# Kernel tuning notes

Measured on AMD Instinct MI355X. Metric: run time of the kernel, lower is better.

## Reference

```python
import jax, jax.numpy as jnp
from jax import lax
import numpy as np
import math

EPS = 1e-5
NBINS = 17   # quantized color levels round(x*255/16) for x in [0,1)
K_MODE = 11

def _bn(x, g, b):
    # BatchNorm2d in training mode: batch statistics over (B,H,W)
    m = jnp.mean(x, axis=(0, 2, 3), keepdims=True)
    v = jnp.var(x, axis=(0, 2, 3), keepdims=True)
    return (x - m) * lax.rsqrt(v + EPS) * g[None, :, None, None] + b[None, :, None, None]

def _lrelu(x):
    return jnp.where(x >= 0, x, 0.01 * x)

def _shared_conv(x, w, b, stride, padding):
    # one KxK kernel shared depthwise across all channels, scalar bias
    C = x.shape[1]
    k = jnp.tile(w[None, None], (C, 1, 1, 1))  # (C,1,K,K)
    y = lax.conv_general_dilated(x, k, (stride, stride),
                                 [(padding, padding), (padding, padding)],
                                 dimension_numbers=('NCHW', 'OIHW', 'NCHW'),
                                 feature_group_count=C)
    return y + b[0]

def _avg_pool_same(x, k):
    # avg_pool2d(k, stride=1, padding=k//2, count_include_pad=True)
    p = k // 2
    s = lax.reduce_window(x, 0.0, lax.add, (1, 1, k, k), (1, 1, 1, 1),
                          [(0, 0), (0, 0), (p, p), (p, p)])
    return s / float(k * k)

def _mode_pool(xq):
    # xq values are exact multiples of 16/256 -> recover integer bin index,
    # then mode over 11x11 window = argmax of per-bin counts (histogram).
    # torch zero-padding corresponds to bin 0; argmax first-max tie-break ->
    # smallest value, matching torch.mode.
    q = jnp.clip(jnp.round(xq * (256.0 / 16.0)).astype(jnp.int32), 0, NBINS - 1)
    pad = K_MODE // 2
    qp = jnp.pad(q, ((0, 0), (0, 0), (pad, pad), (pad, pad)))
    onehot = (qp[:, :, None] == jnp.arange(NBINS, dtype=jnp.int32)[None, None, :, None, None]).astype(jnp.float32)
    counts = lax.reduce_window(onehot, 0.0, lax.add, (1, 1, 1, K_MODE, K_MODE), (1, 1, 1, 1, 1), 'VALID')
    mode_bin = jnp.argmax(counts, axis=2)  # (B,C,H,W)
    return mode_bin.astype(xq.dtype) * (16.0 / 256.0)

def _forward(x, p_w1, p_b1, p_dw1, p_db1, p_g1, p_be1,
             p_w2, p_b2, p_dw2, p_db2, p_g2, p_be2,
             d_w, d_b, ia_w, ia_b, ia_g, ia_be,
             ib_w, ib_b, ib_g, ib_be,
             f_g1, f_be1, f_g2, f_be2):
    xq = jnp.round(x * (255.0 / 16.0)) * (16.0 / 256.0)
    xm = _mode_pool(xq)
    B, C, H, W = xm.shape
    half = p_w1.shape[0]

    # prepare: 1x1 conv -> depthwise 1x1 (per-channel scale) -> BN -> LeakyReLU, twice
    h = jnp.einsum('bchw,oc->bohw', xm, p_w1) + p_b1[None, :, None, None]
    h = h * p_dw1[None, :, None, None] + p_db1[None, :, None, None]
    h = _lrelu(_bn(h, p_g1, p_be1))
    h = jnp.einsum('bchw,oc->bohw', h, p_w2) + p_b2[None, :, None, None]
    h = h * p_dw2[None, :, None, None] + p_db2[None, :, None, None]
    h = _lrelu(_bn(h, p_g2, p_be2))

    n = int(math.floor(math.log(min(H, W), 3)))
    score = jnp.zeros((B, 2 * half, H, W), x.dtype)
    d = h
    for _ in range(n):
        d = _shared_conv(d, d_w, d_b, 3, 1)  # stride-3 downgrade
        z = jax.image.resize(d, (B, half, H, W), method='bilinear')
        a = _lrelu(_bn(_shared_conv(z, ia_w, ia_b, 1, 2), ia_g, ia_be))
        bb = _lrelu(_bn(_shared_conv(z, ib_w, ib_b, 1, 2), ib_g, ib_be))
        score = score + jnp.concatenate([a, bb], axis=1)  # Splitter + Stack(1)

    def ft(s):
        s = _bn(s, f_g1, f_be1)
        s = jnp.where(s > 0.1, 0.1 + 0.7 * (s - 0.1), s)  # MaxLeakyReLU(0.7, 0.1)
        s = _bn(s, f_g2, f_be2)
        return 2.0 * s - _avg_pool_same(s, K_MODE)  # EmphaseLocal(11): x + (x - local mean)

    score = ft(ft(ft(score)))
    return score / n

def setup_inputs() -> dict:
    key = jax.random.key(0)
    ks = jax.random.split(key, 32)
    B, Cin, H, W, half = 8, 3, 384, 384, 32
    r = lambda i, shp, s=0.1: s * jax.random.normal(ks[i], shp, dtype=jnp.float32)
    g = lambda i, shp: 1.0 + 0.1 * jax.random.normal(ks[i], shp, dtype=jnp.float32)
    return dict(
        x=jax.random.uniform(ks[0], (B, Cin, H, W), dtype=jnp.float32),
        p_w1=r(1, (half, Cin), 0.3), p_b1=r(2, (half,)),
        p_dw1=g(3, (half,)), p_db1=r(4, (half,)),
        p_g1=g(5, (half,)), p_be1=r(6, (half,)),
        p_w2=r(7, (half, half), 0.2), p_b2=r(8, (half,)),
        p_dw2=g(9, (half,)), p_db2=r(10, (half,)),
        p_g2=g(11, (half,)), p_be2=r(12, (half,)),
        d_w=r(13, (3, 3), 0.2), d_b=r(14, (1,)),
        ia_w=r(15, (5, 5), 0.2), ia_b=r(16, (1,)),
        ia_g=g(17, (half,)), ia_be=r(18, (half,)),
        ib_w=r(19, (5, 5), 0.2), ib_b=r(20, (1,)),
        ib_g=g(21, (half,)), ib_be=r(22, (half,)),
        f_g1=g(23, (2 * half,)), f_be1=r(24, (2 * half,)),
        f_g2=g(25, (2 * half,)), f_be2=r(26, (2 * half,)),
    )

def reference(x, p_w1, p_b1, p_dw1, p_db1, p_g1, p_be1,
              p_w2, p_b2, p_dw2, p_db2, p_g2, p_be2,
              d_w, d_b, ia_w, ia_b, ia_g, ia_be,
              ib_w, ib_b, ib_g, ib_be,
              f_g1, f_be1, f_g2, f_be2):
    return _forward(x, p_w1, p_b1, p_dw1, p_db1, p_g1, p_be1,
                    p_w2, p_b2, p_dw2, p_db2, p_g2, p_be2,
                    d_w, d_b, ia_w, ia_b, ia_g, ia_be,
                    ib_w, ib_b, ib_g, ib_be,
                    f_g1, f_be1, f_g2, f_be2)
```

## Files before the change

kernel.cpp:

```cpp
#include <hip/hip_runtime.h>

#define HW 147456
#define WID 384
#define NB 8
#define NPC 1179648
#define HW4 36864

static __device__ __forceinline__ float lrelu01(float v) { return v >= 0.f ? v : 0.01f * v; }
static __device__ __forceinline__ float mlrelu(float v) { return v > 0.1f ? 0.1f + 0.7f * (v - 0.1f) : v; }

__global__ __launch_bounds__(256) void mode_kernel(const float* __restrict__ x,
                                                   float* __restrict__ xm) {
  __shared__ unsigned char qt[26 * 76];
  __shared__ unsigned int cc[16 * 5 * 76];
  const int plane = blockIdx.z;
  const int x0 = blockIdx.x * 64;
  const int y0 = blockIdx.y * 16;
  const float* xp = x + (size_t)plane * HW;

  for (int i = threadIdx.x; i < 26 * 76; i += 256) {
    int r = i / 76, ccol = i - r * 76;
    int gy = y0 + r - 5, gx = x0 + ccol - 5;
    unsigned char q = 0;
    if (ccol < 74 && gy >= 0 && gy < WID && gx >= 0 && gx < WID) {
// ... 113 lines not shown
    double e2 = (a0 * a0 * M[3] + a1 * a1 * M[6] + a2 * a2 * M[8] +
                 2.0 * (a0 * a1 * M[4] + a0 * a2 * M[5] + a1 * a2 * M[7])) / N +
                2.0 * k * lin + k * k;
    double var = e2 - mean * mean;
    float rstd = rsqrtf((float)var + 1e-5f);
    float scl = rstd * g[o];
    sc[o] = scl;
    sh[o] = be[o] - (float)mean * scl;
  }
}

__global__ __launch_bounds__(256) void prep_fused(const float* __restrict__ xm,
                                                  const float* __restrict__ w1,
                                                  const float* __restrict__ b1,
                                                  const float* __restrict__ dw1,
                                                  const float* __restrict__ db1,
                                                  const float* __restrict__ P1SC,
                                                  const float* __restrict__ P1SH,
                                                  const float* __restrict__ w2,
                                                  const float* __restrict__ b2,
                                                  const float* __restrict__ dw2,
                                                  const float* __restrict__ db2,
                                                  float* __restrict__ t2,
                                                  float* __restrict__ part) {
  __shared__ float wl[1024];
  __shared__ float c1[32][4];
  __shared__ float bias2[32];
  __shared__ float wred[8][32];
  for (int i = threadIdx.x; i < 1024; i += 256) wl[i] = w2[i] * dw2[i >> 5];
  if (threadIdx.x < 32) {
    int o = threadIdx.x;
    float dw = dw1[o], s1 = P1SC[o];
    c1[o][0] = w1[o * 3] * dw * s1;
    c1[o][1] = w1[o * 3 + 1] * dw * s1;
    c1[o][2] = w1[o * 3 + 2] * dw * s1;
    c1[o][3] = (b1[o] * dw + db1[o]) * s1 + P1SH[o];
    bias2[o] = b2[o] * dw2[o] + db2[o];
  }
  __syncthreads();
  const int p0 = blockIdx.x * 512 + threadIdx.x;
  const int b = p0 / HW, pp = p0 - b * HW;
  const float* xb = xm + (size_t)b * 3 * HW + pp;
  float h[2][32];
#pragma unroll
  for (int q = 0; q < 2; ++q) {
    float x0 = xb[q * 256], x1 = xb[HW + q * 256], x2 = xb[2 * HW + q * 256];
#pragma unroll
    for (int o = 0; o < 32; ++o) {
      float u = fmaf(x0, c1[o][0], fmaf(x1, c1[o][1], fmaf(x2, c1[o][2], c1[o][3])));
      h[q][o] = lrelu01(u);
    }
  }
  float sv[32], sq[32];
  float* ob = t2 + (size_t)b * 32 * HW + pp;
  const float4* wl4 = reinterpret_cast<const float4*>(wl);
  for (int o = 0; o < 32; ++o) {
    float acc0 = bias2[o], acc1 = bias2[o];
#pragma unroll
    for (int c4 = 0; c4 < 8; ++c4) {
      float4 w4 = wl4[o * 8 + c4];
      int c = c4 * 4;
      acc0 = fmaf(h[0][c], w4.x, acc0);     acc1 = fmaf(h[1][c], w4.x, acc1);
      acc0 = fmaf(h[0][c + 1], w4.y, acc0); acc1 = fmaf(h[1][c + 1], w4.y, acc1);
      acc0 = fmaf(h[0][c + 2], w4.z, acc0); acc1 = fmaf(h[1][c + 2], w4.z, acc1);
      acc0 = fmaf(h[0][c + 3], w4.w, acc0); acc1 = fmaf(h[1][c + 3], w4.w, acc1);
    }
    ob[(size_t)o * HW] = acc0;
    ob[(size_t)o * HW + 256] = acc1;
    sv[o] = acc0 + acc1;
    sq[o] = acc0 * acc0 + acc1 * acc1;
  }
  int lane = threadIdx.x & 63, wd = threadIdx.x >> 6;
#pragma unroll
  for (int o = 0; o < 32; ++o) {
    float a = sv[o], q = sq[o];
    for (int off = 32; off; off >>= 1) {
      a += __shfl_down(a, off);
      q += __shfl_down(q, off);
    }
    if (lane == 0) { wred[wd][o] = a; wred[wd + 4][o] = q; }
  }
  __syncthreads();
  if (threadIdx.x < 32) {
    int o = threadIdx.x;
    part[((size_t)o * 2304 + blockIdx.x) * 2] = wred[0][o] + wred[1][o] + wred[2][o] + wred[3][o];
    part[((size_t)o * 2304 + blockIdx.x) * 2 + 1] = wred[4][o] + wred[5][o] + wred[6][o] + wred[7][o];
  }
}

__global__ __launch_bounds__(64) void stats_combine(const float* __restrict__ part, int nsplit,
                                                    const float* __restrict__ g,
                                                    const float* __restrict__ be,
                                                    float* __restrict__ sc,
                                                    float* __restrict__ sh) {
  const int c = blockIdx.x;
  double s = 0.0, q = 0.0;
  for (int i = threadIdx.x; i < nsplit; i += 64) {
    s += part[((size_t)c * nsplit + i) * 2];
    q += part[((size_t)c * nsplit + i) * 2 + 1];
  }
  for (int off = 32; off; off >>= 1) {
    s += __shfl_down(s, off);
    q += __shfl_down(q, off);
  }
  if (threadIdx.x == 0) {
    double mean = s / (double)NPC;
    double var = q / (double)NPC - mean * mean;
    float rstd = rsqrtf((float)var + 1e-5f);
    float scl = rstd * g[c];
    sc[c] = scl;
    sh[c] = be[c] - (float)mean * scl;
  }
}

template <bool AFF>
__global__ __launch_bounds__(256) void dconv(const float* __restrict__ in,
                                             const float* __restrict__ sc,
                                             const float* __restrict__ sh,
                                             const float* __restrict__ w9,
                                             const float* __restrict__ db,
                                             int Sin, int Sout,
                                             float* __restrict__ out, int total) {
  int idx = blockIdx.x * 256 + threadIdx.x;
  if (idx >= total) return;
  int xx = idx % Sout;
  int t = idx / Sout;
  int yy = t % Sout;
  int pc = t / Sout;
  int c = pc & 31;
  const float* ip = in + (size_t)pc * Sin * Sin;
  float a = AFF ? sc[c] : 1.f;
  float h = AFF ? sh[c] : 0.f;
  float acc = 0.f;
#pragma unroll
  for (int ky = 0; ky < 3; ++ky) {
    int iy = 3 * yy - 1 + ky;
    if (iy < 0 || iy >= Sin) continue;
#pragma unroll
    for (int kx = 0; kx < 3; ++kx) {
      int ix = 3 * xx - 1 + kx;
      if (ix < 0 || ix >= Sin) continue;
      float v = ip[(size_t)iy * Sin + ix];
      if (AFF) { v = v * a + h; v = lrelu01(v); }
      acc = fmaf(v, w9[ky * 3 + kx], acc);
    }
  }
  out[idx] = acc + db[0];
}

static __device__ __forceinline__ int sin_of(int l) {
  return l == 0 ? 128 : l == 1 ? 43 : l == 2 ? 15 : l == 3 ? 5 : 2;
}

__device__ __forceinline__ void conv_ab(const float* zt, int row, int g,
                                        const float* wa, const float* wb,
                                        float ba0, float bb0, float* A, float* Bv) {
  float aa0 = ba0, aa1 = ba0, aa2 = ba0, aa3 = ba0;
  float eb0 = bb0, eb1 = bb0, eb2 = bb0, eb3 = bb0;
#pragma unroll
  for (int dy = 0; dy < 5; ++dy) {
    const float* zr = &zt[(row + dy) * 40 + g * 4];
    float4 zlo = *reinterpret_cast<const float4*>(zr);
    float4 zhi = *reinterpret_cast<const float4*>(zr + 4);
    float z[8] = {zlo.x, zlo.y, zlo.z, zlo.w, zhi.x, zhi.y, zhi.z, zhi.w};
#pragma unroll
    for (int dx = 0; dx < 5; ++dx) {
      float wva = wa[dy * 5 + dx], wvb = wb[dy * 5 + dx];
      aa0 = fmaf(z[dx], wva, aa0);
      aa1 = fmaf(z[dx + 1], wva, aa1);
      aa2 = fmaf(z[dx + 2], wva, aa2);
      aa3 = fmaf(z[dx + 3], wva, aa3);
      eb0 = fmaf(z[dx], wvb, eb0);
      eb1 = fmaf(z[dx + 1], wvb, eb1);
      eb2 = fmaf(z[dx + 2], wvb, eb2);
      eb3 = fmaf(z[dx + 3], wvb, eb3);
    }
  }
  A[0] = aa0; A[1] = aa1; A[2] = aa2; A[3] = aa3;
  Bv[0] = eb0; Bv[1] = eb1; Bv[2] = eb2; Bv[3] = eb3;
}

__global__ __launch_bounds__(256) void upstats2(const float* __restrict__ d1,
                                                const float* __restrict__ d2,
                                                const float* __restrict__ d3,
                                                const float* __restrict__ d4,
                                                const float* __restrict__ d5,
                                                const float* __restrict__ wA5,
                                                const float* __restrict__ wB5,
                                                const float* __restrict__ bA,
                                                const float* __restrict__ bB,
                                                float* __restrict__ partA,
                                                float* __restrict__ partB) {
  __shared__ __align__(16) float zt[2][36 * 40];
  __shared__ __align__(16) float dH[2][16 * 40];
  __shared__ int gx0[36], gx1[36], gy0[36], gy1[36];
  __shared__ float gfx[36], gfy[36], gxv[36], gyv[36];
  __shared__ float red[2][16];
  const int lvl = blockIdx.z;
  const float* dsel = lvl == 0 ? d1 : lvl == 1 ? d2 : lvl == 2 ? d3 : lvl == 3 ? d4 : d5;
  const int Sin = sin_of(lvl);
  const float scale = (float)Sin / 384.f;
  const int plane0 = blockIdx.y * 2, tile = blockIdx.x;
  const int tx = (tile % 12) * 32, ty = (tile / 12) * 32;

  if (threadIdx.x < 72) {
    int t = threadIdx.x >= 36 ? threadIdx.x - 36 : threadIdx.x;
    bool isY = threadIdx.x >= 36;
    int gp = (isY ? ty : tx) + t - 2;
    float valid = (gp >= 0 && gp < WID) ? 1.f : 0.f;
    int gpc = gp < 0 ? 0 : (gp >= WID ? WID - 1 : gp);
    float s = (gpc + 0.5f) * scale - 0.5f;
    float f0 = floorf(s);
    float fr = s - f0;
    int ii = (int)f0;
    int i1 = ii + 1 < Sin - 1 ? ii + 1 : Sin - 1;
    int i0 = ii > 0 ? ii : 0;
    if (isY) { gy0[t] = i0; gy1[t] = i1; gfy[t] = fr; gyv[t] = valid; }
    else     { gx0[t] = i0; gx1[t] = i1; gfx[t] = fr; gxv[t] = valid; }
  }
  float wa[25], wb[25];
#pragma unroll
  for (int k = 0; k < 25; ++k) { wa[k] = wA5[k]; wb[k] = wB5[k]; }
  const float ba0 = bA[0], bb0 = bB[0];
  __syncthreads();

  const int rowlo = gy0[0], nrows = gy1[35] - rowlo + 1;
  const int cnt = nrows * 36;
  for (int i = threadIdx.x; i < 2 * cnt; i += 256) {
    int p = i < cnt ? 0 : 1;
    int j = i - p * cnt;
    int r = j / 36, zx = j - r * 36;
    const float* drow = dsel + (size_t)(plane0 + p) * Sin * Sin + (size_t)(rowlo + r) * Sin;
    float v0 = drow[gx0[zx]], v1 = drow[gx1[zx]];
    dH[p][r * 40 + zx] = (v0 + gfx[zx] * (v1 - v0)) * gxv[zx];
  }
  __syncthreads();
  for (int i = threadIdx.x; i < 648; i += 256) {
    int p = i < 324 ? 0 : 1;
    int j = i - p * 324;
    int zy = j / 9, k = j - zy * 9;
    int r0 = gy0[zy] - rowlo, r1 = gy1[zy] - rowlo;
    float fy = gfy[zy], vv = gyv[zy];
    float4 a4 = *reinterpret_cast<const float4*>(&dH[p][r0 * 40 + k * 4]);
    float4 b4 = *reinterpret_cast<const float4*>(&dH[p][r1 * 40 + k * 4]);
    float4 o;
    o.x = (a4.x + fy * (b4.x - a4.x)) * vv;
    o.y = (a4.y + fy * (b4.y - a4.y)) * vv;
    o.z = (a4.z + fy * (b4.z - a4.z)) * vv;
    o.w = (a4.w + fy * (b4.w - a4.w)) * vv;
    *reinterpret_cast<float4*>(&zt[p][zy * 40 + k * 4]) = o;
  }
  __syncthreads();

  const int row = threadIdx.x >> 3, g = threadIdx.x & 7;
  const int lane = threadIdx.x & 63, wd = threadIdx.x >> 6;
#pragma unroll
  for (int p = 0; p < 2; ++p) {
    float A[4], Bv[4];
    conv_ab(zt[p], row, g, wa, wb, ba0, bb0, A, Bv);
    float sa = A[0] + A[1] + A[2] + A[3];
    float qa = A[0] * A[0] + A[1] * A[1] + A[2] * A[2] + A[3] * A[3];
    float sb = Bv[0] + Bv[1] + Bv[2] + Bv[3];
    float qb = Bv[0] * Bv[0] + Bv[1] * Bv[1] + Bv[2] * Bv[2] + Bv[3] * Bv[3];
    for (int off = 32; off; off >>= 1) {
      sa += __shfl_down(sa, off); qa += __shfl_down(qa, off);
      sb += __shfl_down(sb, off); qb += __shfl_down(qb, off);
    }
    if (lane == 0) {
      red[p][wd * 4 + 0] = sa; red[p][wd * 4 + 1] = qa;
      red[p][wd * 4 + 2] = sb; red[p][wd * 4 + 3] = qb;
    }
  }
  __syncthreads();
  if (threadIdx.x < 2) {
    int p = threadIdx.x;
    int plane = plane0 + p;
    int b = plane >> 5, c = plane & 31;
    const float* r_ = red[p];
    size_t pi = (size_t)lvl * 73728 + ((size_t)c * 1152 + (size_t)b * 144 + tile) * 2;
    partA[pi] = r_[0] + r_[4] + r_[8] + r_[12];
    partA[pi + 1] = r_[1] + r_[5] + r_[9] + r_[13];
    partB[pi] = r_[2] + r_[6] + r_[10] + r_[14];
    partB[pi + 1] = r_[3] + r_[7] + r_[11] + r_[15];
  }
}

__global__ __launch_bounds__(64) void combine_lvls(const float* __restrict__ partA,
                                                   const float* __restrict__ partB,
                                                   const float* __restrict__ ia_g,
                                                   const float* __restrict__ ia_be,
                                                   const float* __restrict__ ib_g,
                                                   const float* __restrict__ ib_be,
                                                   float* __restrict__ aff) {
  const int c = blockIdx.x, lvl = blockIdx.y, z = blockIdx.z;
  const float* part = (z ? partB : partA) + (size_t)lvl * 73728;
  const float* g = z ? ib_g : ia_g;
  const float* be = z ? ib_be : ia_be;
  double s = 0.0, q = 0.0;
  for (int i = threadIdx.x; i < 1152; i += 64) {
    s += part[((size_t)c * 1152 + i) * 2];
    q += part[((size_t)c * 1152 + i) * 2 + 1];
  }
  for (int off = 32; off; off >>= 1) {
    s += __shfl_down(s, off);
    q += __shfl_down(q, off);
  }
  if (threadIdx.x == 0) {
    double mean = s / (double)NPC;
    double var = q / (double)NPC - mean * mean;
    float rstd = rsqrtf((float)var + 1e-5f);
    float scl = rstd * g[c];
    aff[((z * 5 + lvl) * 2 + 0) * 32 + c] = scl;
    aff[((z * 5 + lvl) * 2 + 1) * 32 + c] = be[c] - (float)mean * scl;
  }
}

__global__ __launch_bounds__(256) void apply_all(const float* __restrict__ d1,
                                                 const float* __restrict__ d2,
                                                 const float* __restrict__ d3,
                                                 const float* __restrict__ d4,
                                                 const float* __restrict__ d5,
                                                 const float* __restrict__ wA5,
                                                 const float* __restrict__ wB5,
                                                 const float* __restrict__ bA,
                                                 const float* __restrict__ bB,
                                                 const float* __restrict__ aff,
                                                 float* __restrict__ outp,
                                                 float* __restrict__ partF) {
  __shared__ __align__(16) float zt[36 * 40];
  __shared__ __align__(16) float dH[16 * 40];
  __shared__ int gx0[5][36], gx1[5][36], gy0[5][36], gy1[5][36];
  __shared__ float gfx[5][36], gfy[5][36], gxv[5][36], gyv[5][36];
  __shared__ float red[16];
  const int plane = blockIdx.y, tile = blockIdx.x;
  const int tx = (tile % 12) * 32, ty = (tile / 12) * 32;
  const int b = plane >> 5, c = plane & 31;
  float wa[25], wb[25];
#pragma unroll
  for (int k = 0; k < 25; ++k) { wa[k] = wA5[k]; wb[k] = wB5[k]; }
  const float ba0 = bA[0], bb0 = bB[0];
  const int row = threadIdx.x >> 3, g = threadIdx.x & 7;

  for (int i = threadIdx.x; i < 360; i += 256) {
    int l = i / 72, j = i - l * 72;
    int t = j >= 36 ? j - 36 : j;
    bool isY = j >= 36;
    int Sin = sin_of(l);
    float scale = (float)Sin / 384.f;
    int gp = (isY ? ty : tx) + t - 2;
    float valid = (gp >= 0 && gp < WID) ? 1.f : 0.f;
    int gpc = gp < 0 ? 0 : (gp >= WID ? WID - 1 : gp);
    float s = (gpc + 0.5f) * scale - 0.5f;
    float f0 = floorf(s);
    float fr = s - f0;
    int ii = (int)f0;
    int i1 = ii + 1 < Sin - 1 ? ii + 1 : Sin - 1;
    int i0 = ii > 0 ? ii : 0;
    if (isY) { gy0[l][t] = i0; gy1[l][t] = i1; gfy[l][t] = fr; gyv[l][t] = valid; }
    else     { gx0[l][t] = i0; gx1[l][t] = i1; gfx[l][t] = fr; gxv[l][t] = valid; }
  }
  __syncthreads();

  float acA[4] = {0.f, 0.f, 0.f, 0.f}, acB[4] = {0.f, 0.f, 0.f, 0.f};
  for (int l = 0; l < 5; ++l) {
    const float* dsel = l == 0 ? d1 : l == 1 ? d2 : l == 2 ? d3 : l == 3 ? d4 : d5;
    const int Sin = sin_of(l);
    const float* dp = dsel + (size_t)plane * Sin * Sin;
    const int rowlo = gy0[l][0], nrows = gy1[l][35] - rowlo + 1;
    for (int i = threadIdx.x; i < nrows * 36; i += 256) {
      int r = i / 36, zx = i - r * 36;
      const float* drow = dp + (size_t)(rowlo + r) * Sin;
      float v0 = drow[gx0[l][zx]], v1 = drow[gx1[l][zx]];
      dH[r * 40 + zx] = (v0 + gfx[l][zx] * (v1 - v0)) * gxv[l][zx];
    }
    __syncthreads();
    for (int i = threadIdx.x; i < 324; i += 256) {
      int zy = i / 9, k = i - zy * 9;
      int r0 = gy0[l][zy] - rowlo, r1 = gy1[l][zy] - rowlo;
      float fy = gfy[l][zy], vv = gyv[l][zy];
      float4 a4 = *reinterpret_cast<const float4*>(&dH[r0 * 40 + k * 4]);
      float4 b4 = *reinterpret_cast<const float4*>(&dH[r1 * 40 + k * 4]);
      float4 o;
      o.x = (a4.x + fy * (b4.x - a4.x)) * vv;
      o.y = (a4.y + fy * (b4.y - a4.y)) * vv;
      o.z = (a4.z + fy * (b4.z - a4.z)) * vv;
      o.w = (a4.w + fy * (b4.w - a4.w)) * vv;
      *reinterpret_cast<float4*>(&zt[zy * 40 + k * 4]) = o;
    }
    __syncthreads();
    float A[4], Bv[4];
    conv_ab(zt, row, g, wa, wb, ba0, bb0, A, Bv);
    float as = aff[(l * 2 + 0) * 32 + c], ah = aff[(l * 2 + 1) * 32 + c];
    float bs = aff[((5 + l) * 2 + 0) * 32 + c], bh = aff[((5 + l) * 2 + 1) * 32 + c];
#pragma unroll
    for (int j = 0; j < 4; ++j) {
      acA[j] += lrelu01(fmaf(A[j], as, ah));
      acB[j] += lrelu01(fmaf(Bv[j], bs, bh));
    }
  }
  float4 xa = {acA[0], acA[1], acA[2], acA[3]};
  float4 xb = {acB[0], acB[1], acB[2], acB[3]};
  size_t po = (size_t)(b * 64 + c) * HW + (size_t)(ty + row) * WID + tx + g * 4;
  *reinterpret_cast<float4*>(outp + po) = xa;
  *reinterpret_cast<float4*>(outp + po + (size_t)32 * HW) = xb;

  float sa = xa.x + xa.y + xa.z + xa.w;
  float qa = xa.x * xa.x + xa.y * xa.y + xa.z * xa.z + xa.w * xa.w;
  float sb = xb.x + xb.y + xb.z + xb.w;
  float qb = xb.x * xb.x + xb.y * xb.y + xb.z * xb.z + xb.w * xb.w;
  int lane = threadIdx.x & 63, wd = threadIdx.x >> 6;
  for (int off = 32; off; off >>= 1) {
    sa += __shfl_down(sa, off); qa += __shfl_down(qa, off);
    sb += __shfl_down(sb, off); qb += __shfl_down(qb, off);
  }
  __syncthreads();
  if (lane == 0) {
    red[wd * 4 + 0] = sa; red[wd * 4 + 1] = qa;
    red[wd * 4 + 2] = sb; red[wd * 4 + 3] = qb;
  }
  __syncthreads();
  if (threadIdx.x == 0) {
    size_t piA = ((size_t)c * 1152 + (size_t)b * 144 + tile) * 2;
    size_t piB = ((size_t)(c + 32) * 1152 + (size_t)b * 144 + tile) * 2;
    partF[piA] = red[0] + red[4] + red[8] + red[12];
    partF[piA + 1] = red[1] + red[5] + red[9] + red[13];
    partF[piB] = red[2] + red[6] + red[10] + red[14];
    partF[piB + 1] = red[3] + red[7] + red[11] + red[15];
  }
}

__global__ __launch_bounds__(256) void stats_mlrelu(const float4* __restrict__ X,
                                                    const float* __restrict__ sc1,
                                                    const float* __restrict__ sh1,
                                                    float* __restrict__ part) {
  int c = blockIdx.x >> 6, s = blockIdx.x & 63;
  float a1 = sc1[c], b1 = sh1[c];
  float sum = 0.f, sq = 0.f;
  int b = s >> 3;
  const float4* Xp = X + (size_t)(b * 64 + c) * HW4 + (s & 7) * 4608 + threadIdx.x;
#pragma unroll 6
  for (int it = 0; it < 18; ++it) {
    float4 v = Xp[it * 256];
    float u;
    u = mlrelu(fmaf(v.x, a1, b1)); sum += u; sq += u * u;
    u = mlrelu(fmaf(v.y, a1, b1)); sum += u; sq += u * u;
    u = mlrelu(fmaf(v.z, a1, b1)); sum += u; sq += u * u;
    u = mlrelu(fmaf(v.w, a1, b1)); sum += u; sq += u * u;
  }
  int lane = threadIdx.x & 63, wd = threadIdx.x >> 6;
  for (int off = 32; off; off >>= 1) {
    sum += __shfl_down(sum, off);
    sq += __shfl_down(sq, off);
  }
  __shared__ float red[8];
  if (lane == 0) { red[wd * 2] = sum; red[wd * 2 + 1] = sq; }
  __syncthreads();
  if (threadIdx.x == 0) {
    part[((size_t)c * 64 + s) * 2] = red[0] + red[2] + red[4] + red[6];
    part[((size_t)c * 64 + s) * 2 + 1] = red[1] + red[3] + red[5] + red[7];
  }
}

__global__ __launch_bounds__(256) void ft_fused(const float* __restrict__ src,
                                                const float* __restrict__ F1SC,
                                                const float* __restrict__ F1SH,
                                                const float* __restrict__ F2SC,
                                                const float* __restrict__ F2SH,
                                                float* __restrict__ dst, float fscale,
                                                float* __restrict__ part) {
  __shared__ float sl[74 * 81];
  __shared__ __align__(16) float Hl[74 * 64];
  __shared__ float red[8];
  const int tile = blockIdx.x;
  const int plane = blockIdx.y;
  const int b = plane >> 6, c = plane & 63;
  const int tx = (tile % 6) * 64, ty = (tile / 6) * 64;
  const float a1 = F1SC[c], b1 = F1SH[c], a2 = F2SC[c], b2 = F2SH[c];
  const float* sp = src + (size_t)plane * HW;

  for (int i = threadIdx.x; i < 74 * 20; i += 256) {
    int r = i / 20, k = i - r * 20;
    int gy = ty + r - 5, gx = tx + k * 4 - 8;
    float4 sv = {0.f, 0.f, 0.f, 0.f};
    if (gy >= 0 && gy < WID && gx >= 0 && gx < WID) {
      float4 v = *reinterpret_cast<const float4*>(sp + (size_t)gy * WID + gx);
      sv.x = fmaf(mlrelu(fmaf(v.x, a1, b1)), a2, b2);
      sv.y = fmaf(mlrelu(fmaf(v.y, a1, b1)), a2, b2);
      sv.z = fmaf(mlrelu(fmaf(v.z, a1, b1)), a2, b2);
      sv.w = fmaf(mlrelu(fmaf(v.w, a1, b1)), a2, b2);
    }
    int base = r * 81 + k * 4;
    sl[base] = sv.x; sl[base + 1] = sv.y; sl[base + 2] = sv.z; sl[base + 3] = sv.w;
  }
  __syncthreads();

  for (int i = threadIdx.x; i < 74 * 16; i += 256) {
    int r = i >> 4, g = i & 15;
    const float* s0 = &sl[r * 81 + g * 4 + 3];
    float v[14];
#pragma unroll
    for (int j = 0; j < 14; ++j) v[j] = s0[j];
    float h0 = v[0] + v[1] + v[2] + v[3] + v[4] + v[5] + v[6] + v[7] + v[8] + v[9] + v[10];
    float h1 = h0 - v[0] + v[11];
    float h2 = h1 - v[1] + v[12];
    float h3 = h2 - v[2] + v[13];
    float4 hh = {h0, h1, h2, h3};
    *reinterpret_cast<float4*>(&Hl[r * 64 + g * 4]) = hh;
  }
  __syncthreads();

  const int g = threadIdx.x & 15, ly = threadIdx.x >> 4;
  const int y0 = ly * 4;
  const float4* H4 = reinterpret_cast<const float4*>(Hl);
  float4 acc = H4[y0 * 16 + g];
#pragma unroll
  for (int dy = 1; dy < 11; ++dy) {
    float4 t = H4[(y0 + dy) * 16 + g];
    acc.x += t.x; acc.y += t.y; acc.z += t.z; acc.w += t.w;
  }
  float sum = 0.f, sq = 0.f;
  float* dpo = dst + (size_t)plane * HW;
#pragma unroll
  for (int ry = 0; ry < 4; ++ry) {
    int y = y0 + ry;
    if (ry) {
      float4 ta = H4[(y + 10) * 16 + g];
      float4 tb = H4[(y - 1) * 16 + g];
      acc.x += ta.x - tb.x; acc.y += ta.y - tb.y;
      acc.z += ta.z - tb.z; acc.w += ta.w - tb.w;
    }
    const float* cp = &sl[(y + 5) * 81 + g * 4 + 8];
    float4 o;
    o.x = (2.f * cp[0] - acc.x * (1.f / 121.f)) * fscale;
    o.y = (2.f * cp[1] - acc.y * (1.f / 121.f)) * fscale;
    o.z = (2.f * cp[2] - acc.z * (1.f / 121.f)) * fscale;
    o.w = (2.f * cp[3] - acc.w * (1.f / 121.f)) * fscale;
    *reinterpret_cast<float4*>(dpo + (size_t)(ty + y) * WID + tx + g * 4) = o;
    sum += o.x + o.y + o.z + o.w;
    sq += o.x * o.x + o.y * o.y + o.z * o.z + o.w * o.w;
  }
  if (part) {
    int lane = threadIdx.x & 63, wd = threadIdx.x >> 6;
    for (int off = 32; off; off >>= 1) {
      sum += __shfl_down(sum, off);
      sq += __shfl_down(sq, off);
    }
    if (lane == 0) { red[wd * 2] = sum; red[wd * 2 + 1] = sq; }
    __syncthreads();
    if (threadIdx.x == 0) {
      size_t pi = ((size_t)c * 288 + (size_t)b * 36 + tile) * 2;
      part[pi] = red[0] + red[2] + red[4] + red[6];
      part[pi + 1] = red[1] + red[3] + red[5] + red[7];
    }
  }
}

extern "C" void kernel_launch(void* const* d_in, const int* in_sizes, int n_in,
                              void* d_out, int out_size, void* d_ws, size_t ws_size,
                              hipStream_t stream) {
  const float* x     = (const float*)d_in[0];
  const float* p_w1  = (const float*)d_in[1];
  const float* p_b1  = (const float*)d_in[2];
  const float* p_dw1 = (const float*)d_in[3];
  const float* p_db1 = (const float*)d_in[4];
  const float* p_g1  = (const float*)d_in[5];
  const float* p_be1 = (const float*)d_in[6];
  const float* p_w2  = (const float*)d_in[7];
  const float* p_b2  = (const float*)d_in[8];
  const float* p_dw2 = (const float*)d_in[9];
  const float* p_db2 = (const float*)d_in[10];
  const float* p_g2  = (const float*)d_in[11];
  const float* p_be2 = (const float*)d_in[12];
  const float* d_w   = (const float*)d_in[13];
  const float* d_b   = (const float*)d_in[14];
  const float* ia_w  = (const float*)d_in[15];
  const float* ia_b  = (const float*)d_in[16];
  const float* ia_g  = (const float*)d_in[17];
  const float* ia_be = (const float*)d_in[18];
  const float* ib_w  = (const float*)d_in[19];
  const float* ib_b  = (const float*)d_in[20];
  const float* ib_g  = (const float*)d_in[21];
  const float* ib_be = (const float*)d_in[22];
  const float* f_g1  = (const float*)d_in[23];
  const float* f_be1 = (const float*)d_in[24];
  const float* f_g2  = (const float*)d_in[25];
  const float* f_be2 = (const float*)d_in[26];
  float* out = (float*)d_out;
  float* ws = (float*)d_ws;

  const size_t SLOT = 37748736ull;
  float* B0 = ws;
  float* B1 = ws + 2 * SLOT;
  float* t2 = B0;
  float* partA = B0 + SLOT;
  float* partB = partA + 368640;
  float* partP = partB + 368640;
  float* part9 = partP + 147456;
  float* aff   = part9 + 2304;
  float* xm  = B1;
  float* dd1 = xm + 3538944;
  float* dd2 = dd1 + 4194304;
  float* dd3 = dd2 + 473344;
  float* dd4 = dd3 + 57600;
  float* dd5 = dd4 + 6400;
  float* partF = ws + 4 * SLOT;
  float* partS = partF + 147456;
  float* st    = partS + 8192;

  float* P1SC = st,       *P1SH = st + 32;
  float* P2SC = st + 64,  *P2SH = st + 96;
  float* F1SC = st + 128, *F1SH = st + 192;
  float* F2SC = st + 256, *F2SH = st + 320;

  mode_kernel<<<dim3(6, 24, 24), 256, 0, stream>>>(x, xm);
  xm_mom<<<256, 256, 0, stream>>>((const float4*)xm, part9);
  prep1_affine<<<1, 64, 0, stream>>>(part9, p_w1, p_b1, p_dw1, p_db1, p_g1, p_be1, P1SC, P1SH);
  prep_fused<<<2304, 256, 0, stream>>>(xm, p_w1, p_b1, p_dw1, p_db1, P1SC, P1SH,
                                       p_w2, p_b2, p_dw2, p_db2, t2, partP);
  stats_combine<<<32, 64, 0, stream>>>(partP, 2304, p_g2, p_be2, P2SC, P2SH);

  dconv<true><<<16384, 256, 0, stream>>>(t2, P2SC, P2SH, d_w, d_b, 384, 128, dd1,
                                         8 * 32 * 128 * 128);
  dconv<false><<<(8 * 32 * 43 * 43 + 255) / 256, 256, 0, stream>>>(
      dd1, nullptr, nullptr, d_w, d_b, 128, 43, dd2, 8 * 32 * 43 * 43);
  dconv<false><<<(8 * 32 * 15 * 15 + 255) / 256, 256, 0, stream>>>(
      dd2, nullptr, nullptr, d_w, d_b, 43, 15, dd3, 8 * 32 * 15 * 15);
  dconv<false><<<(8 * 32 * 5 * 5 + 255) / 256, 256, 0, stream>>>(
      dd3, nullptr, nullptr, d_w, d_b, 15, 5, dd4, 8 * 32 * 5 * 5);
  dconv<false><<<(8 * 32 * 2 * 2 + 255) / 256, 256, 0, stream>>>(
      dd4, nullptr, nullptr, d_w, d_b, 5, 2, dd5, 8 * 32 * 2 * 2);

  upstats2<<<dim3(144, 128, 5), 256, 0, stream>>>(dd1, dd2, dd3, dd4, dd5,
                                                  ia_w, ib_w, ia_b, ib_b, partA, partB);
  combine_lvls<<<dim3(32, 5, 2), 64, 0, stream>>>(partA, partB, ia_g, ia_be, ib_g, ib_be, aff);
  apply_all<<<dim3(144, 256), 256, 0, stream>>>(dd1, dd2, dd3, dd4, dd5,
                                                ia_w, ib_w, ia_b, ib_b, aff, out, partF);

  const float* cur = out;
  float* dsts[3] = {B0, B1, out};
  for (int k = 0; k < 3; ++k) {
    stats_combine<<<64, 64, 0, stream>>>(partF, (k == 0) ? 1152 : 288, f_g1, f_be1, F1SC, F1SH);
    stats_mlrelu<<<64 * 64, 256, 0, stream>>>((const float4*)cur, F1SC, F1SH, partS);
    stats_combine<<<64, 64, 0, stream>>>(partS, 64, f_g2, f_be2, F2SC, F2SH);
    ft_fused<<<dim3(36, 512), 256, 0, stream>>>(cur, F1SC, F1SH, F2SC, F2SH, dsts[k],
                                                (k == 2) ? 0.2f : 1.0f,
                                                (k < 2) ? partF : nullptr);
    cur = dsts[k];
  }
}
```

Measured before the change: 2.097 ms.

## Use 32x64 tiles with two-row conv per thread and precomputed resize geometry

The upsample+conv stats and apply kernels now process 32x64 output tiles instead of 32x32. Each thread computes two adjacent output rows, reusing the loaded input rows across the shared 5x5 taps. Bilinear resize indices and fractions are computed once into a global geometry table rather than per block. This halves block count and the halo overhead per output. Partial-stat layouts and the combine kernels are resized to match, with slightly more register pressure per thread.

```diff
diff --git a/kernel.cpp b/kernel.cpp
--- a/kernel.cpp
+++ b/kernel.cpp
@@ -289,116 +289,144 @@
   return l == 0 ? 128 : l == 1 ? 43 : l == 2 ? 15 : l == 3 ? 5 : 2;
 }
 
-__device__ __forceinline__ void conv_ab(const float* zt, int row, int g,
-                                        const float* wa, const float* wb,
-                                        float ba0, float bb0, float* A, float* Bv) {
-  float aa0 = ba0, aa1 = ba0, aa2 = ba0, aa3 = ba0;
-  float eb0 = bb0, eb1 = bb0, eb2 = bb0, eb3 = bb0;
-#pragma unroll
-  for (int dy = 0; dy < 5; ++dy) {
-    const float* zr = &zt[(row + dy) * 40 + g * 4];
-    float4 zlo = *reinterpret_cast<const float4*>(zr);
-    float4 zhi = *reinterpret_cast<const float4*>(zr + 4);
+__global__ __launch_bounds__(256) void geo_build(float4* __restrict__ geo) {
+  int id = blockIdx.x * 256 + threadIdx.x;
+  if (id >= 5 * 384) return;
+  int l = id / 384, p = id - l * 384;
+  int Sin = sin_of(l);
+  float scale = (float)Sin / 384.f;
+  float s = (p + 0.5f) * scale - 0.5f;
+  float f0 = floorf(s);
+  float fr = s - f0;
+  int ii = (int)f0;
+  int i1 = ii + 1 < Sin - 1 ? ii + 1 : Sin - 1;
+  int i0 = ii > 0 ? ii : 0;
+  geo[id] = make_float4((float)i0, (float)i1, fr, 0.f);
+}
+
+static __device__ __forceinline__ int clamp383(int v) {
+  return v < 0 ? 0 : (v > 383 ? 383 : v);
+}
+
+__device__ __forceinline__ void conv2row(const float* zt, int u, int g,
+                                         const float* wa, const float* wb,
+                                         float ba0, float bb0,
+                                         float* A0, float* A1, float* B0, float* B1) {
+#pragma unroll
+  for (int j = 0; j < 4; ++j) { A0[j] = ba0; A1[j] = ba0; B0[j] = bb0; B1[j] = bb0; }
+  const float* zp = zt + (2 * u) * 72 + g * 4;
+#pragma unroll
+  for (int zr = 0; zr < 6; ++zr) {
+    float4 zlo = *reinterpret_cast<const float4*>(zp + zr * 72);
+    float4 zhi = *reinterpret_cast<const float4*>(zp + zr * 72 + 4);
     float z[8] = {zlo.x, zlo.y, zlo.z, zlo.w, zhi.x, zhi.y, zhi.z, zhi.w};
-#pragma unroll
-    for (int dx = 0; dx < 5; ++dx) {
-      float wva = wa[dy * 5 + dx], wvb = wb[dy * 5 + dx];
-      aa0 = fmaf(z[dx], wva, aa0);
-      aa1 = fmaf(z[dx + 1], wva, aa1);
-      aa2 = fmaf(z[dx + 2], wva, aa2);
-      aa3 = fmaf(z[dx + 3], wva, aa3);
-      eb0 = fmaf(z[dx], wvb, eb0);
-      eb1 = fmaf(z[dx + 1], wvb, eb1);
-      eb2 = fmaf(z[dx + 2], wvb, eb2);
-      eb3 = fmaf(z[dx + 3], wvb, eb3);
-    }
-  }
-  A[0] = aa0; A[1] = aa1; A[2] = aa2; A[3] = aa3;
-  Bv[0] = eb0; Bv[1] = eb1; Bv[2] = eb2; Bv[3] = eb3;
-}
-
-__global__ __launch_bounds__(256) void upstats2(const float* __restrict__ d1,
-                                                const float* __restrict__ d2,
-                                                const float* __restrict__ d3,
-                                                const float* __restrict__ d4,
-                                                const float* __restrict__ d5,
-                                                const float* __restrict__ wA5,
-                                                const float* __restrict__ wB5,
-                                                const float* __restrict__ bA,
-                                                const float* __restrict__ bB,
-                                                float* __restrict__ partA,
-                                                float* __restrict__ partB) {
-  __shared__ __align__(16) float zt[2][36 * 40];
-  __shared__ __align__(16) float dH[2][16 * 40];
-  __shared__ int gx0[36], gx1[36], gy0[36], gy1[36];
-  __shared__ float gfx[36], gfy[36], gxv[36], gyv[36];
+    if (zr < 5) {
+#pragma unroll
+      for (int dx = 0; dx < 5; ++dx) {
+        float wva = wa[zr * 5 + dx], wvb = wb[zr * 5 + dx];
+#pragma unroll
+        for (int j = 0; j < 4; ++j) {
+          A0[j] = fmaf(z[dx + j], wva, A0[j]);
+          B0[j] = fmaf(z[dx + j], wvb, B0[j]);
+        }
+      }
+    }
+    if (zr >= 1) {
+#pragma unroll
+      for (int dx = 0; dx < 5; ++dx) {
+        float wva = wa[(zr - 1) * 5 + dx], wvb = wb[(zr - 1) * 5 + dx];
+#pragma unroll
+        for (int j = 0; j < 4; ++j) {
+          A1[j] = fmaf(z[dx + j], wva, A1[j]);
+          B1[j] = fmaf(z[dx + j], wvb, B1[j]);
+        }
+      }
+    }
+  }
+}
+
+__global__ __launch_bounds__(256) void upstats64(const float* __restrict__ d1,
+                                                 const float* __restrict__ d2,
+                                                 const float* __restrict__ d3,
+                                                 const float* __restrict__ d4,
+                                                 const float* __restrict__ d5,
+                                                 const float4* __restrict__ geo,
+                                                 const float* __restrict__ wA5,
+                                                 const float* __restrict__ wB5,
+                                                 const float* __restrict__ bA,
+                                                 const float* __restrict__ bB,
+                                                 float* __restrict__ partA,
+                                                 float* __restrict__ partB) {
+  __shared__ __align__(16) float zt[2][36 * 72];
+  __shared__ __align__(16) float dH[2][16 * 72];
   __shared__ float red[2][16];
   const int lvl = blockIdx.z;
   const float* dsel = lvl == 0 ? d1 : lvl == 1 ? d2 : lvl == 2 ? d3 : lvl == 3 ? d4 : d5;
   const int Sin = sin_of(lvl);
-  const float scale = (float)Sin / 384.f;
   const int plane0 = blockIdx.y * 2, tile = blockIdx.x;
-  const int tx = (tile % 12) * 32, ty = (tile / 12) * 32;
-
-  if (threadIdx.x < 72) {
-    int t = threadIdx.x >= 36 ? threadIdx.x - 36 : threadIdx.x;
-    bool isY = threadIdx.x >= 36;
-    int gp = (isY ? ty : tx) + t - 2;
-    float valid = (gp >= 0 && gp < WID) ? 1.f : 0.f;
-    int gpc = gp < 0 ? 0 : (gp >= WID ? WID - 1 : gp);
-    float s = (gpc + 0.5f) * scale - 0.5f;
-    float f0 = floorf(s);
-    float fr = s - f0;
-    int ii = (int)f0;
-    int i1 = ii + 1 < Sin - 1 ? ii + 1 : Sin - 1;
-    int i0 = ii > 0 ? ii : 0;
-    if (isY) { gy0[t] = i0; gy1[t] = i1; gfy[t] = fr; gyv[t] = valid; }
-    else     { gx0[t] = i0; gx1[t] = i1; gfx[t] = fr; gxv[t] = valid; }
-  }
+  const int tx = (tile % 6) * 64, ty = (tile / 6) * 32;
+  const float4* xg = geo + lvl * 384;
+  const float* dp0 = dsel + (size_t)plane0 * Sin * Sin;
+  const float* dp1 = dp0 + Sin * Sin;
+
   float wa[25], wb[25];
 #pragma unroll
   for (int k = 0; k < 25; ++k) { wa[k] = wA5[k]; wb[k] = wB5[k]; }
   const float ba0 = bA[0], bb0 = bB[0];
-  __syncthreads();
-
-  const int rowlo = gy0[0], nrows = gy1[35] - rowlo + 1;
-  const int cnt = nrows * 36;
+
+  const int rowlo = (int)xg[clamp383(ty - 2)].x;
+  const int rowhi = (int)xg[clamp383(ty + 33)].y;
+  const int nr = rowhi - rowlo + 1;
+  const int cnt = nr * 68;
+
   for (int i = threadIdx.x; i < 2 * cnt; i += 256) {
     int p = i < cnt ? 0 : 1;
     int j = i - p * cnt;
-    int r = j / 36, zx = j - r * 36;
-    const float* drow = dsel + (size_t)(plane0 + p) * Sin * Sin + (size_t)(rowlo + r) * Sin;
-    float v0 = drow[gx0[zx]], v1 = drow[gx1[zx]];
-    dH[p][r * 40 + zx] = (v0 + gfx[zx] * (v1 - v0)) * gxv[zx];
-  }
-  __syncthreads();
-  for (int i = threadIdx.x; i < 648; i += 256) {
-    int p = i < 324 ? 0 : 1;
-    int j = i - p * 324;
-    int zy = j / 9, k = j - zy * 9;
-    int r0 = gy0[zy] - rowlo, r1 = gy1[zy] - rowlo;
-    float fy = gfy[zy], vv = gyv[zy];
-    float4 a4 = *reinterpret_cast<const float4*>(&dH[p][r0 * 40 + k * 4]);
-    float4 b4 = *reinterpret_cast<const float4*>(&dH[p][r1 * 40 + k * 4]);
+    int r = j / 68, zx = j - r * 68;
+    int gp = tx + zx - 2;
+    int gpc = clamp383(gp);
+    float vd = (gp == gpc) ? 1.f : 0.f;
+    float4 ge = xg[gpc];
+    const float* drow = (p ? dp1 : dp0) + (size_t)(rowlo + r) * Sin;
+    float v0 = drow[(int)ge.x], v1 = drow[(int)ge.y];
+    dH[p][r * 72 + zx] = (v0 + ge.z * (v1 - v0)) * vd;
+  }
+  __syncthreads();
+  for (int i = threadIdx.x; i < 2 * 612; i += 256) {
+    int p = i < 612 ? 0 : 1;
+    int j = i - p * 612;
+    int zy = j / 17, k = j - zy * 17;
+    int gp = ty + zy - 2;
+    int gpc = clamp383(gp);
+    float vd = (gp == gpc) ? 1.f : 0.f;
+    float4 ge = xg[gpc];
+    int r0 = (int)ge.x - rowlo, r1 = (int)ge.y - rowlo;
+    float fy = ge.z;
+    float4 a4 = *reinterpret_cast<const float4*>(&dH[p][r0 * 72 + k * 4]);
+    float4 b4 = *reinterpret_cast<const float4*>(&dH[p][r1 * 72 + k * 4]);
     float4 o;
-    o.x = (a4.x + fy * (b4.x - a4.x)) * vv;
-    o.y = (a4.y + fy * (b4.y - a4.y)) * vv;
-    o.z = (a4.z + fy * (b4.z - a4.z)) * vv;
-    o.w = (a4.w + fy * (b4.w - a4.w)) * vv;
-    *reinterpret_cast<float4*>(&zt[p][zy * 40 + k * 4]) = o;
-  }
-  __syncthreads();
-
-  const int row = threadIdx.x >> 3, g = threadIdx.x & 7;
+    o.x = (a4.x + fy * (b4.x - a4.x)) * vd;
+    o.y = (a4.y + fy * (b4.y - a4.y)) * vd;
+    o.z = (a4.z + fy * (b4.z - a4.z)) * vd;
+    o.w = (a4.w + fy * (b4.w - a4.w)) * vd;
+    *reinterpret_cast<float4*>(&zt[p][zy * 72 + k * 4]) = o;
+  }
+  __syncthreads();
+
+  const int u = threadIdx.x >> 4, g = threadIdx.x & 15;
   const int lane = threadIdx.x & 63, wd = threadIdx.x >> 6;
 #pragma unroll
   for (int p = 0; p < 2; ++p) {
-    float A[4], Bv[4];
-    conv_ab(zt[p], row, g, wa, wb, ba0, bb0, A, Bv);
-    float sa = A[0] + A[1] + A[2] + A[3];
-    float qa = A[0] * A[0] + A[1] * A[1] + A[2] * A[2] + A[3] * A[3];
-    float sb = Bv[0] + Bv[1] + Bv[2] + Bv[3];
-    float qb = Bv[0] * Bv[0] + Bv[1] * Bv[1] + Bv[2] * Bv[2] + Bv[3] * Bv[3];
+    float A0[4], A1[4], B0[4], B1[4];
+    conv2row(zt[p], u, g, wa, wb, ba0, bb0, A0, A1, B0, B1);
+    float sa = 0.f, qa = 0.f, sb = 0.f, qb = 0.f;
+#pragma unroll
+    for (int j = 0; j < 4; ++j) {
+      sa += A0[j] + A1[j];
+      qa += A0[j] * A0[j] + A1[j] * A1[j];
+      sb += B0[j] + B1[j];
+      qb += B0[j] * B0[j] + B1[j] * B1[j];
+    }
     for (int off = 32; off; off >>= 1) {
       sa += __shfl_down(sa, off); qa += __shfl_down(qa, off);
       sb += __shfl_down(sb, off); qb += __shfl_down(qb, off);
@@ -414,7 +442,7 @@
     int plane = plane0 + p;
     int b = plane >> 5, c = plane & 31;
     const float* r_ = red[p];
-    size_t pi = (size_t)lvl * 73728 + ((size_t)c * 1152 + (size_t)b * 144 + tile) * 2;
+    size_t pi = ((size_t)lvl * 32 + c) * 576 * 2 + ((size_t)b * 72 + tile) * 2;
     partA[pi] = r_[0] + r_[4] + r_[8] + r_[12];
     partA[pi + 1] = r_[1] + r_[5] + r_[9] + r_[13];
     partB[pi] = r_[2] + r_[6] + r_[10] + r_[14];
@@ -430,13 +458,13 @@
                                                    const float* __restrict__ ib_be,
                                                    float* __restrict__ aff) {
   const int c = blockIdx.x, lvl = blockIdx.y, z = blockIdx.z;
-  const float* part = (z ? partB : partA) + (size_t)lvl * 73728;
+  const float* part = (z ? partB : partA) + (size_t)lvl * 32 * 576 * 2;
   const float* g = z ? ib_g : ia_g;
   const float* be = z ? ib_be : ia_be;
   double s = 0.0, q = 0.0;
-  for (int i = threadIdx.x; i < 1152; i += 64) {
-    s += part[((size_t)c * 1152 + i) * 2];
-    q += part[((size_t)c * 1152 + i) * 2 + 1];
+  for (int i = threadIdx.x; i < 576; i += 64) {
+    s += part[((size_t)c * 576 + i) * 2];
+    q += part[((size_t)c * 576 + i) * 2 + 1];
   }
   for (int off = 32; off; off >>= 1) {
     s += __shfl_down(s, off);
@@ -452,113 +480,115 @@
   }
 }
 
-__global__ __launch_bounds__(256) void apply_all(const float* __restrict__ d1,
-                                                 const float* __restrict__ d2,
-                                                 const float* __restrict__ d3,
-                                                 const float* __restrict__ d4,
-                                                 const float* __restrict__ d5,
-                                                 const float* __restrict__ wA5,
-                                                 const float* __restrict__ wB5,
-                                                 const float* __restrict__ bA,
-                                                 const float* __restrict__ bB,
-                                                 const float* __restrict__ aff,
-                                                 float* __restrict__ outp,
-                                                 float* __restrict__ partF) {
-  __shared__ __align__(16) float zt[36 * 40];
-  __shared__ __align__(16) float dH[16 * 40];
-  __shared__ int gx0[5][36], gx1[5][36], gy0[5][36], gy1[5][36];
-  __shared__ float gfx[5][36], gfy[5][36], gxv[5][36], gyv[5][36];
+__global__ __launch_bounds__(256) void apply64(const float* __restrict__ d1,
+                                               const float* __restrict__ d2,
+                                               const float* __restrict__ d3,
+                                               const float* __restrict__ d4,
+                                               const float* __restrict__ d5,
+                                               const float4* __restrict__ geo,
+                                               const float* __restrict__ wA5,
+                                               const float* __restrict__ wB5,
+                                               const float* __restrict__ bA,
+                                               const float* __restrict__ bB,
+                                               const float* __restrict__ aff,
+                                               float* __restrict__ outp,
+                                               float* __restrict__ partF) {
+  __shared__ __align__(16) float zt[36 * 72];
+  __shared__ __align__(16) float dH[16 * 72];
   __shared__ float red[16];
   const int plane = blockIdx.y, tile = blockIdx.x;
-  const int tx = (tile % 12) * 32, ty = (tile / 12) * 32;
+  const int tx = (tile % 6) * 64, ty = (tile / 6) * 32;
   const int b = plane >> 5, c = plane & 31;
   float wa[25], wb[25];
 #pragma unroll
   for (int k = 0; k < 25; ++k) { wa[k] = wA5[k]; wb[k] = wB5[k]; }
   const float ba0 = bA[0], bb0 = bB[0];
-  const int row = threadIdx.x >> 3, g = threadIdx.x & 7;
-
-  for (int i = threadIdx.x; i < 360; i += 256) {
-    int l = i / 72, j = i - l * 72;
-    int t = j >= 36 ? j - 36 : j;
-    bool isY = j >= 36;
-    int Sin = sin_of(l);
-    float scale = (float)Sin / 384.f;
-    int gp = (isY ? ty : tx) + t - 2;
-    float valid = (gp >= 0 && gp < WID) ? 1.f : 0.f;
-    int gpc = gp < 0 ? 0 : (gp >= WID ? WID - 1 : gp);
-    float s = (gpc + 0.5f) * scale - 0.5f;
-    float f0 = floorf(s);
-    float fr = s - f0;
-    int ii = (int)f0;
-    int i1 = ii + 1 < Sin - 1 ? ii + 1 : Sin - 1;
-    int i0 = ii > 0 ? ii : 0;
-    if (isY) { gy0[l][t] = i0; gy1[l][t] = i1; gfy[l][t] = fr; gyv[l][t] = valid; }
-    else     { gx0[l][t] = i0; gx1[l][t] = i1; gfx[l][t] = fr; gxv[l][t] = valid; }
-  }
-  __syncthreads();
-
-  float acA[4] = {0.f, 0.f, 0.f, 0.f}, acB[4] = {0.f, 0.f, 0.f, 0.f};
+  const int u = threadIdx.x >> 4, g = threadIdx.x & 15;
+
+  float acA0[4] = {0, 0, 0, 0}, acA1[4] = {0, 0, 0, 0};
+  float acB0[4] = {0, 0, 0, 0}, acB1[4] = {0, 0, 0, 0};
+
   for (int l = 0; l < 5; ++l) {
     const float* dsel = l == 0 ? d1 : l == 1 ? d2 : l == 2 ? d3 : l == 3 ? d4 : d5;
     const int Sin = sin_of(l);
     const float* dp = dsel + (size_t)plane * Sin * Sin;
-    const int rowlo = gy0[l][0], nrows = gy1[l][35] - rowlo + 1;
-    for (int i = threadIdx.x; i < nrows * 36; i += 256) {
-      int r = i / 36, zx = i - r * 36;
+    const float4* xg = geo + l * 384;
+    const int rowlo = (int)xg[clamp383(ty - 2)].x;
+    const int rowhi = (int)xg[clamp383(ty + 33)].y;
+    const int nr = rowhi - rowlo + 1;
+    for (int i = threadIdx.x; i < nr * 68; i += 256) {
+      int r = i / 68, zx = i - r * 68;
+      int gp = tx + zx - 2;
+      int gpc = clamp383(gp);
+      float vd = (gp == gpc) ? 1.f : 0.f;
+      float4 ge = xg[gpc];
       const float* drow = dp + (size_t)(rowlo + r) * Sin;
-      float v0 = drow[gx0[l][zx]], v1 = drow[gx1[l][zx]];
-      dH[r * 40 + zx] = (v0 + gfx[l][zx] * (v1 - v0)) * gxv[l][zx];
+      float v0 = drow[(int)ge.x], v1 = drow[(int)ge.y];
+      dH[r * 72 + zx] = (v0 + ge.z * (v1 - v0)) * vd;
     }
     __syncthreads();
-    for (int i = threadIdx.x; i < 324; i += 256) {
-      int zy = i / 9, k = i - zy * 9;
-      int r0 = gy0[l][zy] - rowlo, r1 = gy1[l][zy] - rowlo;
-      float fy = gfy[l][zy], vv = gyv[l][zy];
-      float4 a4 = *reinterpret_cast<const float4*>(&dH[r0 * 40 + k * 4]);
-      float4 b4 = *reinterpret_cast<const float4*>(&dH[r1 * 40 + k * 4]);
+    for (int i = threadIdx.x; i < 612; i += 256) {
+      int zy = i / 17, k = i - zy * 17;
+      int gp = ty + zy - 2;
+      int gpc = clamp383(gp);
+      float vd = (gp == gpc) ? 1.f : 0.f;
+      float4 ge = xg[gpc];
+      int r0 = (int)ge.x - rowlo, r1 = (int)ge.y - rowlo;
+      float fy = ge.z;
+      float4 a4 = *reinterpret_cast<const float4*>(&dH[r0 * 72 + k * 4]);
+      float4 b4 = *reinterpret_cast<const float4*>(&dH[r1 * 72 + k * 4]);
       float4 o;
-      o.x = (a4.x + fy * (b4.x - a4.x)) * vv;
-      o.y = (a4.y + fy * (b4.y - a4.y)) * vv;
-      o.z = (a4.z + fy * (b4.z - a4.z)) * vv;
-      o.w = (a4.w + fy * (b4.w - a4.w)) * vv;
-      *reinterpret_cast<float4*>(&zt[zy * 40 + k * 4]) = o;
+      o.x = (a4.x + fy * (b4.x - a4.x)) * vd;
+      o.y = (a4.y + fy * (b4.y - a4.y)) * vd;
+      o.z = (a4.z + fy * (b4.z - a4.z)) * vd;
+      o.w = (a4.w + fy * (b4.w - a4.w)) * vd;
+      *reinterpret_cast<float4*>(&zt[zy * 72 + k * 4]) = o;
     }
     __syncthreads();
-    float A[4], Bv[4];
-    conv_ab(zt, row, g, wa, wb, ba0, bb0, A, Bv);
+    float A0[4], A1[4], B0[4], B1[4];
+    conv2row(zt, u, g, wa, wb, ba0, bb0, A0, A1, B0, B1);
     float as = aff[(l * 2 + 0) * 32 + c], ah = aff[(l * 2 + 1) * 32 + c];
     float bs = aff[((5 + l) * 2 + 0) * 32 + c], bh = aff[((5 + l) * 2 + 1) * 32 + c];
 #pragma unroll
     for (int j = 0; j < 4; ++j) {
-      acA[j] += lrelu01(fmaf(A[j], as, ah));
-      acB[j] += lrelu01(fmaf(Bv[j], bs, bh));
-    }
-  }
-  float4 xa = {acA[0], acA[1], acA[2], acA[3]};
-  float4 xb = {acB[0], acB[1], acB[2], acB[3]};
-  size_t po = (size_t)(b * 64 + c) * HW + (size_t)(ty + row) * WID + tx + g * 4;
-  *reinterpret_cast<float4*>(outp + po) = xa;
-  *reinterpret_cast<float4*>(outp + po + (size_t)32 * HW) = xb;
-
-  float sa = xa.x + xa.y + xa.z + xa.w;
-  float qa = xa.x * xa.x + xa.y * xa.y + xa.z * xa.z + xa.w * xa.w;
-  float sb = xb.x + xb.y + xb.z + xb.w;
-  float qb = xb.x * xb.x + xb.y * xb.y + xb.z * xb.z + xb.w * xb.w;
+      acA0[j] += lrelu01(fmaf(A0[j], as, ah));
+      acA1[j] += lrelu01(fmaf(A1[j], as, ah));
+      acB0[j] += lrelu01(fmaf(B0[j], bs, bh));
+      acB1[j] += lrelu01(fmaf(B1[j], bs, bh));
+    }
+  }
+
+  float4 xa0 = {acA0[0], acA0[1], acA0[2], acA0[3]};
+  float4 xa1 = {acA1[0], acA1[1], acA1[2], acA1[3]};
+  float4 xb0 = {acB0[0], acB0[1], acB0[2], acB0[3]};
+  float4 xb1 = {acB1[0], acB1[1], acB1[2], acB1[3]};
+  size_t po = (size_t)(b * 64 + c) * HW + (size_t)(ty + 2 * u) * WID + tx + g * 4;
+  *reinterpret_cast<float4*>(outp + po) = xa0;
+  *reinterpret_cast<float4*>(outp + po + WID) = xa1;
+  *reinterpret_cast<float4*>(outp + po + (size_t)32 * HW) = xb0;
+  *reinterpret_cast<float4*>(outp + po + (size_t)32 * HW + WID) = xb1;
+
+  float sa = 0.f, qa = 0.f, sb = 0.f, qb = 0.f;
+#pragma unroll
+  for (int j = 0; j < 4; ++j) {
+    sa += acA0[j] + acA1[j];
+    qa += acA0[j] * acA0[j] + acA1[j] * acA1[j];
+    sb += acB0[j] + acB1[j];
+    qb += acB0[j] * acB0[j] + acB1[j] * acB1[j];
+  }
   int lane = threadIdx.x & 63, wd = threadIdx.x >> 6;
   for (int off = 32; off; off >>= 1) {
     sa += __shfl_down(sa, off); qa += __shfl_down(qa, off);
     sb += __shfl_down(sb, off); qb += __shfl_down(qb, off);
   }
-  __syncthreads();
   if (lane == 0) {
     red[wd * 4 + 0] = sa; red[wd * 4 + 1] = qa;
     red[wd * 4 + 2] = sb; red[wd * 4 + 3] = qb;
   }
   __syncthreads();
   if (threadIdx.x == 0) {
-    size_t piA = ((size_t)c * 1152 + (size_t)b * 144 + tile) * 2;
-    size_t piB = ((size_t)(c + 32) * 1152 + (size_t)b * 144 + tile) * 2;
+    size_t piA = ((size_t)c * 576 + (size_t)b * 72 + tile) * 2;
+    size_t piB = ((size_t)(c + 32) * 576 + (size_t)b * 72 + tile) * 2;
     partF[piA] = red[0] + red[4] + red[8] + red[12];
     partF[piA + 1] = red[1] + red[5] + red[9] + red[13];
     partF[piB] = red[2] + red[6] + red[10] + red[14];
@@ -743,12 +773,14 @@
   float* partF = ws + 4 * SLOT;
   float* partS = partF + 147456;
   float* st    = partS + 8192;
+  float* geoT  = st + 512;
 
   float* P1SC = st,       *P1SH = st + 32;
   float* P2SC = st + 64,  *P2SH = st + 96;
   float* F1SC = st + 128, *F1SH = st + 192;
   float* F2SC = st + 256, *F2SH = st + 320;
 
+  geo_build<<<8, 256, 0, stream>>>((float4*)geoT);
   mode_kernel<<<dim3(6, 24, 24), 256, 0, stream>>>(x, xm);
   xm_mom<<<256, 256, 0, stream>>>((const float4*)xm, part9);
   prep1_affine<<<1, 64, 0, stream>>>(part9, p_w1, p_b1, p_dw1, p_db1, p_g1, p_be1, P1SC, P1SH);
@@ -767,16 +799,18 @@
   dconv<false><<<(8 * 32 * 2 * 2 + 255) / 256, 256, 0, stream>>>(
       dd4, nullptr, nullptr, d_w, d_b, 5, 2, dd5, 8 * 32 * 2 * 2);
 
-  upstats2<<<dim3(144, 128, 5), 256, 0, stream>>>(dd1, dd2, dd3, dd4, dd5,
+  upstats64<<<dim3(72, 128, 5), 256, 0, stream>>>(dd1, dd2, dd3, dd4, dd5,
+                                                  (const float4*)geoT,
                                                   ia_w, ib_w, ia_b, ib_b, partA, partB);
   combine_lvls<<<dim3(32, 5, 2), 64, 0, stream>>>(partA, partB, ia_g, ia_be, ib_g, ib_be, aff);
-  apply_all<<<dim3(144, 256), 256, 0, stream>>>(dd1, dd2, dd3, dd4, dd5,
-                                                ia_w, ib_w, ia_b, ib_b, aff, out, partF);
+  apply64<<<dim3(72, 256), 256, 0, stream>>>(dd1, dd2, dd3, dd4, dd5,
+                                             (const float4*)geoT,
+                                             ia_w, ib_w, ia_b, ib_b, aff, out, partF);
 
   const float* cur = out;
   float* dsts[3] = {B0, B1, out};
   for (int k = 0; k < 3; ++k) {
-    stats_combine<<<64, 64, 0, stream>>>(partF, (k == 0) ? 1152 : 288, f_g1, f_be1, F1SC, F1SH);
+    stats_combine<<<64, 64, 0, stream>>>(partF, (k == 0) ? 576 : 288, f_g1, f_be1, F1SC, F1SH);
     stats_mlrelu<<<64 * 64, 256, 0, stream>>>((const float4*)cur, F1SC, F1SH, partS);
     stats_combine<<<64, 64, 0, stream>>>(partS, 64, f_g2, f_be2, F2SC, F2SH);
     ft_fused<<<dim3(36, 512), 256, 0, stream>>>(cur, F1SC, F1SH, F2SC, F2SH, dsts[k],
```

Result: faster. 1.815 ms (-13.5%).
